# Optimization experiments

Measured on AMD Instinct MI355X. Metric: run time of the kernel, lower is better.

## Reference

```python
import jax, jax.numpy as jnp
import numpy as np

NUM_HEADS = 8
LN_EPS = 1e-5


def _avg_pool_mat(n_in, n_out):
    # torch adaptive_avg_pool windows: start=floor(i*n_in/n_out), end=ceil((i+1)*n_in/n_out)
    M = np.zeros((n_out, n_in), dtype=np.float32)
    for i in range(n_out):
        s = (i * n_in) // n_out
        e = -((-(i + 1) * n_in) // n_out)
        M[i, s:e] = 1.0 / (e - s)
    return jnp.asarray(M)


def _adaptive_avg_pool(x, out_hw):
    # separable mean over rectangular windows: [B,C,H,W] -> [B,C,out,out]
    Mh = _avg_pool_mat(x.shape[2], out_hw)
    Mw = _avg_pool_mat(x.shape[3], out_hw)
    return jnp.einsum('bchw,ph,qw->bcpq', x, Mh, Mw)


def _max_pool(x, oh, ow):
    # exact (divisible) adaptive max pool
    B, C, H, W = x.shape
    assert H % oh == 0 and W % ow == 0
    return x.reshape(B, C, oh, H // oh, ow, W // ow).max(axis=(3, 5))


def _conv1x1_res(t, w, b):
    # t + Conv2d(1x1)(t); w is [C_in, C_out]
    return t + jnp.einsum('bchw,cd->bdhw', t, w) + b[None, :, None, None]


def _tokens(t):
    B, C = t.shape[:2]
    return t.reshape(B, C, -1).transpose(0, 2, 1)  # [B, hw, C]


def setup_inputs():
    B, L, C = 8, 1024, 512
    H = W = 64
    key = jax.random.key(0)
    ks = jax.random.split(key, 16)
    n = lambda k, s, sc=0.02: jax.random.normal(k, s, jnp.float32) * sc
    return dict(
        x=jax.random.normal(ks[0], (B, H * W, C), jnp.float32),
        m=jax.random.normal(ks[1], (B, L, C), jnp.float32),
        w_s1=n(ks[2], (C, C)), b_s1=n(ks[3], (C,)),
        w_s2=n(ks[4], (C, C)), b_s2=n(ks[5], (C,)),
        w_s3=n(ks[6], (C, C)), b_s3=n(ks[7], (C,)),
        w_s4=n(ks[8], (C, C)), b_s4=n(ks[9], (C,)),
        w_mx=n(ks[10], (C, C)), b_mx=n(ks[11], (C,)),
        ln_g=jnp.ones((C,), jnp.float32), ln_b=jnp.zeros((C,), jnp.float32),
        Wq=n(ks[12], (C, C)), Wkv=n(ks[13], (C, 2 * C)),
        Wp=n(ks[14], (C, C)), bp=n(ks[15], (C,)),
        H=H, W=W, patch_size=16,
    )


def reference(x, m, w_s1, b_s1, w_s2, b_s2, w_s3, b_s3, w_s4, b_s4,
              w_mx, b_mx, ln_g, ln_b, Wq, Wkv, Wp, bp, H, W, patch_size):
    B, L, C = m.shape
    nh = NUM_HEADS
    d = C // nh
    scale = d ** -0.5

    q = (m @ Wq).reshape(B, L, nh, d).transpose(0, 2, 1, 3)  # [B,nh,L,d]

    x_ = x.transpose(0, 2, 1).reshape(B, C, H, W)
    s1 = _conv1x1_res(_adaptive_avg_pool(x_, round(H * 4 / 12)), w_s1, b_s1)
    s2 = _conv1x1_res(_adaptive_avg_pool(x_, round(H * 4 / 16)), w_s2, b_s2)
    s3 = _conv1x1_res(_adaptive_avg_pool(x_, round(H * 4 / 20)), w_s3, b_s3)
    s4 = _conv1x1_res(_adaptive_avg_pool(x_, round(H * 4 / 24)), w_s4, b_s4)
    mx = _conv1x1_res(_max_pool(x_, H * 4 // patch_size, W * 4 // patch_size), w_mx, b_mx)

    p = jnp.concatenate([_tokens(s1), _tokens(s2), _tokens(s3), _tokens(s4), _tokens(mx)], axis=1)
    mu = p.mean(-1, keepdims=True)
    var = ((p - mu) ** 2).mean(-1, keepdims=True)
    p = (p - mu) / jnp.sqrt(var + LN_EPS) * ln_g + ln_b

    kv_in = jnp.concatenate([p, m], axis=1)  # [B, N_p+L, C]
    kv = (kv_in @ Wkv).reshape(B, -1, 2, nh, d)
    k = kv[:, :, 0].transpose(0, 2, 1, 3)  # [B,nh,N,d]
    v = kv[:, :, 1].transpose(0, 2, 1, 3)

    attn = jax.nn.softmax(jnp.einsum('bhld,bhnd->bhln', q, k) * scale, axis=-1)
    out = jnp.einsum('bhln,bhnd->bhld', attn, v).transpose(0, 2, 1, 3).reshape(B, L, C)
    out = out @ Wp + bp
    return out, mx
```

## Files before the change

### kernel.cpp

```cpp
#include <hip/hip_runtime.h>

typedef unsigned short u16;
typedef __attribute__((ext_vector_type(8))) short bf16x8;
typedef __attribute__((ext_vector_type(4))) float f32x4;
typedef __attribute__((ext_vector_type(16))) float f32x16;
typedef int i32x2 __attribute__((ext_vector_type(2)));

__device__ __forceinline__ float bf2f(u16 u) {
  union { unsigned int i; float f; } x; x.i = ((unsigned int)u) << 16; return x.f;
}
__device__ __forceinline__ u16 f2bf(float f) {
  union { float f; unsigned int i; } x; x.f = f;
  unsigned int r = x.i + 0x7fffu + ((x.i >> 16) & 1u);
  return (u16)(r >> 16);
}

#define CFENCE() asm volatile("" ::: "memory")

__device__ __forceinline__ unsigned cvtpk_bf16(float lo, float hi) {
  unsigned r;
  asm("v_cvt_pk_bf16_f32 %0, %1, %2" : "=v"(r) : "v"(lo), "v"(hi));
  return r;
}

__global__ __launch_bounds__(256) void k_pool(
    const float* __restrict__ x, u16* __restrict__ pool,
    const float* __restrict__ m, u16* __restrict__ mb)
{
  int blk = blockIdx.x;
  if (blk >= 9944) {
    size_t i = ((size_t)(blk - 9944) * 256 + threadIdx.x) * 8;
    float4 a = *(const float4*)(m + i);
    float4 b = *(const float4*)(m + i + 4);
    ushort4 u0, u1;
    u0.x = f2bf(a.x); u0.y = f2bf(a.y); u0.z = f2bf(a.z); u0.w = f2bf(a.w);
    u1.x = f2bf(b.x); u1.y = f2bf(b.y); u1.z = f2bf(b.z); u1.w = f2bf(b.w);
    *(ushort4*)(mb + i) = u0;
    *(ushort4*)(mb + i + 4) = u1;
    return;
  }
  int b = blk / 1243;
  int tok = blk - b * 1243;
  int c = threadIdx.x;
  const float* xb = x + (size_t)b * 4096 * 512;
  float r0, r1;
  if (tok >= 987) {
    int t = tok - 987;
    int oh = t >> 4, ow = t & 15;
    float m0 = -1e38f, m1 = -1e38f;
    for (int hh = 0; hh < 4; hh++)
      for (int ww = 0; ww < 4; ww++) {
        const float* px = xb + (size_t)((oh * 4 + hh) * 64 + ow * 4 + ww) * 512 + c;
        m0 = fmaxf(m0, px[0]);
        m1 = fmaxf(m1, px[256]);
      }
    r0 = m0; r1 = m1;
  } else {
    int n, t;
    if (tok < 441)      { n = 21; t = tok; }
    else if (tok < 697) { n = 16; t = tok - 441; }
    else if (tok < 866) { n = 13; t = tok - 697; }
    else                { n = 11; t = tok - 866; }
    int oh = t / n, ow = t - oh * n;
    int h0 = (oh * 64) / n, h1 = ((oh + 1) * 64 + n - 1) / n;
    int w0 = (ow * 64) / n, w1 = ((ow + 1) * 64 + n - 1) / n;
    float inv = 1.0f / (float)((h1 - h0) * (w1 - w0));
    float s0 = 0.f, s1 = 0.f;
    for (int hh = h0; hh < h1; hh++)
      for (int ww = w0; ww < w1; ww++) {
        const float* px = xb + (size_t)(hh * 64 + ww) * 512 + c;
        s0 += px[0];
        s1 += px[256];
      }
    r0 = s0 * inv; r1 = s1 * inv;
  }
  u16* dst = pool + (size_t)(b * 1243 + tok) * 512 + c;
  dst[0]   = f2bf(r0);
  dst[256] = f2bf(r1);
}

__global__ __launch_bounds__(256) void k_wt8(
    const float* w0, const float* w1, const float* w2, const float* w3,
    const float* w4, const float* w5, const float* w6, const float* w7,
    u16* __restrict__ wt_base)
{
  int z = blockIdx.z;
  int N = (z == 6) ? 1024 : 512;
  if (N == 512 && blockIdx.x >= 16) return;
  const float* W =
      z == 0 ? w0 : z == 1 ? w1 : z == 2 ? w2 : z == 3 ? w3 :
      z == 4 ? w4 : z == 5 ? w5 : z == 6 ? w6 : w7;
  size_t doff = (z <= 5) ? (size_t)z * 262144
                         : (z == 6 ? (size_t)6 * 262144 : (size_t)6 * 262144 + 524288);
  u16* Wt = wt_base + doff;

  __shared__ float tile[32][33];
  int n0 = blockIdx.x * 32, k0 = blockIdx.y * 32;
  int t = threadIdx.x;
  int rr = t >> 5, cc = t & 31;
#pragma unroll
  for (int ps = 0; ps < 4; ps++)
    tile[ps * 8 + rr][cc] = W[(size_t)(k0 + ps * 8 + rr) * N + n0 + cc];
  __syncthreads();
#pragma unroll
  for (int ps = 0; ps < 4; ps++)
    Wt[(size_t)(n0 + ps * 8 + rr) * 512 + k0 + cc] = f2bf(tile[cc][ps * 8 + rr]);
}

template <class EPI>
__device__ __forceinline__ void gemm_core(
    const u16* __restrict__ Az, const u16* __restrict__ Bt,
    int M, int K, int m0, int n0, EPI&& epi)
{
  __shared__ __align__(16) u16 As[128][40];
  __shared__ __align__(16) u16 Bs[128][40];

  const int tid = threadIdx.x;
  const int lane = tid & 63, wv = tid >> 6;
  const int quad = lane >> 4, l15 = lane & 15;
  const int wm = (wv >> 1) * 64, wn = (wv & 1) * 64;

  f32x4 acc[4][4];
#pragma unroll
  for (int i = 0; i < 4; i++)
#pragma unroll
    for (int j = 0; j < 4; j++) acc[i][j] = (f32x4){0.f, 0.f, 0.f, 0.f};

  const int srow = tid >> 1;
  const int scol = (tid & 1) * 16;
  const bool aok = (m0 + srow) < M;
  const u16* ag = Az + (size_t)(m0 + srow) * K + scol;
  const u16* bg = Bt + (size_t)(n0 + srow) * K + scol;

  uint4 a0 = {0, 0, 0, 0}, a1 = {0, 0, 0, 0}, b0, b1;
  if (aok) { a0 = *(const uint4*)ag; a1 = *(const uint4*)(ag + 8); }
  b0 = *(const uint4*)bg;
  b1 = *(const uint4*)(bg + 8);

  for (int k0 = 0; k0 < K; k0 += 32) {
    CFENCE();
    __builtin_amdgcn_s_barrier();
    asm volatile("s_waitcnt vmcnt(0)" ::: "memory");
    *(uint4*)&As[srow][scol]     = a0;
    *(uint4*)&As[srow][scol + 8] = a1;
    *(uint4*)&Bs[srow][scol]     = b0;
    *(uint4*)&Bs[srow][scol + 8] = b1;
    if (k0 + 32 < K) {
      if (aok) { a0 = *(const uint4*)(ag + k0 + 32); a1 = *(const uint4*)(ag + k0 + 40); }
      b0 = *(const uint4*)(bg + k0 + 32);
      b1 = *(const uint4*)(bg + k0 + 40);
    }
    asm volatile("s_waitcnt lgkmcnt(0)" ::: "memory");
    __builtin_amdgcn_s_barrier();
    CFENCE();

    bf16x8 af[4];
#pragma unroll
    for (int i = 0; i < 4; i++)
      af[i] = *(const bf16x8*)&As[wm + i * 16 + l15][quad * 8];
#pragma unroll
    for (int j = 0; j < 4; j++) {
      bf16x8 bfj = *(const bf16x8*)&Bs[wn + j * 16 + l15][quad * 8];
#pragma unroll
      for (int i = 0; i < 4; i++)
        acc[i][j] = __builtin_amdgcn_mfma_f32_16x16x32_bf16(af[i], bfj, acc[i][j], 0, 0, 0);
    }
  }

#pragma unroll
  for (int i = 0; i < 4; i++) {
    int rb = m0 + wm + i * 16 + quad * 4;
#pragma unroll
    for (int j = 0; j < 4; j++) {
      int col = n0 + wn + j * 16 + l15;
#pragma unroll
      for (int r = 0; r < 4; r++) {
        int row = rb + r;
        if (row >= M) continue;
        epi(row, col, acc[i][j][r]);
      }
    }
  }
}

__global__ __launch_bounds__(256) void k_gemm_f32(
    const u16* __restrict__ A, long long a_bs, const u16* __restrict__ Bt,
    const float* __restrict__ bias, float* __restrict__ C, long long c_bs,
    int M, int N, int K)
{
  const u16* Az = A + (size_t)blockIdx.z * a_bs;
  float* Cz = C + (size_t)blockIdx.z * c_bs;
  gemm_core(Az, Bt, M, K, blockIdx.y * 128, blockIdx.x * 128,
            [&](int row, int col, float v) {
              Cz[(size_t)row * N + col] = v + bias[col];
            });
}

__global__ __launch_bounds__(256) void k_gemm_big(
    const u16* __restrict__ mb, const u16* __restrict__ p,
    const u16* __restrict__ wqkv, const u16* __restrict__ wkv,
    u16* __restrict__ q, u16* __restrict__ KV)
{
  int y = blockIdx.y, z = blockIdx.z;
  if (y < 8) {
    const u16* Az = mb + (size_t)z * (1024 * 512);
    u16* qz  = q  + (size_t)z * (1024 * 512);
    u16* kvz = KV + (size_t)(z * 2267 + 1243) * 1024;
    gemm_core(Az, wqkv, 1024, 512, y * 128, blockIdx.x * 128,
              [&](int row, int col, float v) {
                u16 bv = f2bf(v);
                if (col < 512) qz[(size_t)row * 512 + col] = bv;
                else           kvz[(size_t)row * 1024 + (col - 512)] = bv;
              });
  } else {
    if (blockIdx.x >= 8) return;
    const u16* Az = p + (size_t)z * (1243 * 512);
    u16* kvz = KV + (size_t)z * 2267 * 1024;
    gemm_core(Az, wkv, 1243, 512, (y - 8) * 128, blockIdx.x * 128,
              [&](int row, int col, float v) {
                kvz[(size_t)row * 1024 + col] = f2bf(v);
              });
  }
}

__global__ __launch_bounds__(256) void k_conv_seg(
    const u16* __restrict__ pool, const u16* __restrict__ wts,
    const float* b0, const float* b1, const float* b2, const float* b3,
    const float* b4, u16* __restrict__ p, float* __restrict__ out2)
{
  int y = blockIdx.y, bz = blockIdx.z;
  int s, m0;
  if (y < 4)      { s = 0; m0 = y * 128; }
  else if (y < 6) { s = 1; m0 = (y - 4) * 128; }
  else if (y < 8) { s = 2; m0 = (y - 6) * 128; }
  else if (y < 9) { s = 3; m0 = 0; }
  else            { s = 4; m0 = (y - 9) * 128; }
  int t0  = s == 0 ? 0 : s == 1 ? 441 : s == 2 ? 697 : s == 3 ? 866 : 987;
  int cnt = s == 0 ? 441 : s == 1 ? 256 : s == 2 ? 169 : s == 3 ? 121 : 256;
  const float* bias = s == 0 ? b0 : s == 1 ? b1 : s == 2 ? b2 : s == 3 ? b3 : b4;
  size_t base = (size_t)bz * (1243 * 512) + (size_t)t0 * 512;
  const u16* Az = pool + base;
  u16* Cz = p + base;
  gemm_core(Az, wts + (size_t)s * 262144, cnt, 512, m0, blockIdx.x * 128,
            [&](int row, int col, float v) {
              v += bias[col] + bf2f(Az[(size_t)row * 512 + col]);
              Cz[(size_t)row * 512 + col] = f2bf(v);
              if (s == 4)
                out2[((size_t)(bz * 512 + col)) * 256 + row] = v;
            });
}

__global__ __launch_bounds__(256) void k_ln(
    u16* __restrict__ p, const float* __restrict__ g, const float* __restrict__ bb)
{
  __shared__ float red[8];
  size_t row = blockIdx.x;
  u16* pr = p + row * 512;
  int t = threadIdx.x;
  float v0 = bf2f(pr[t]), v1 = bf2f(pr[t + 256]);
  float s = v0 + v1;
#pragma unroll
  for (int off = 1; off < 64; off <<= 1) s += __shfl_xor(s, off);
  int wave = t >> 6;
  if ((t & 63) == 0) red[wave] = s;
  __syncthreads();
  float mean = (red[0] + red[1] + red[2] + red[3]) * (1.f / 512.f);
  float d0 = v0 - mean, d1 = v1 - mean;
  float s2 = d0 * d0 + d1 * d1;
#pragma unroll
  for (int off = 1; off < 64; off <<= 1) s2 += __shfl_xor(s2, off);
  if ((t & 63) == 0) red[4 + wave] = s2;
  __syncthreads();
  float var = (red[4] + red[5] + red[6] + red[7]) * (1.f / 512.f);
  float rstd = rsqrtf(var + 1e-5f);
  pr[t]       = f2bf(d0 * rstd * g[t]       + bb[t]);
  pr[t + 256] = f2bf(d1 * rstd * g[t + 256] + bb[t + 256]);
}

__global__ __launch_bounds__(256) void k_attn_mfma(
    const u16* __restrict__ qb, const u16* __restrict__ KV,
    u16* __restrict__ outb)
{
  __shared__ __align__(16) u16 Ks_[64][68];
  __shared__ __align__(16) u16 Vt_[64][68];

  const int bid = blockIdx.x;
  const int qt = bid >> 6;
  const int hb = bid & 63;
  const int h = hb & 7, b = hb >> 3;
  const int tid = threadIdx.x;
  const int lane = tid & 63, wv = tid >> 6;
  const int l31 = lane & 31, hl = lane >> 5;

  const u16* kvb = KV + (size_t)b * 2267 * 1024;
  const int kr = tid >> 2, kc = (tid & 3) * 16;
  const int vp = tid & 31, vo = tid >> 5;

  uint4 k0r = {0,0,0,0}, k1r = {0,0,0,0}, vra = {0,0,0,0}, vrb = {0,0,0,0};
  auto load_tile = [&](int n0) {
    k0r = (uint4){0,0,0,0}; k1r = (uint4){0,0,0,0};
    vra = (uint4){0,0,0,0}; vrb = (uint4){0,0,0,0};
    if (n0 + kr < 2267) {
      const u16* s = kvb + (size_t)(n0 + kr) * 1024 + h * 64 + kc;
      k0r = *(const uint4*)s;
      k1r = *(const uint4*)(s + 8);
    }
    int na = n0 + 2 * vp;
    const u16* s = kvb + (size_t)na * 1024 + 512 + h * 64 + vo * 8;
    if (na < 2267)     vra = *(const uint4*)s;
    if (na + 1 < 2267) vrb = *(const uint4*)(s + 1024);
  };

  load_tile(0);
  bf16x8 qf[4];
  {
    const u16* qrow = qb + (size_t)(b * 1024 + qt * 128 + wv * 32 + l31) * 512
                    + h * 64 + hl * 8;
    qf[0] = *(const bf16x8*)(qrow);
    qf[1] = *(const bf16x8*)(qrow + 16);
    qf[2] = *(const bf16x8*)(qrow + 32);
    qf[3] = *(const bf16x8*)(qrow + 48);
  }

  float l_acc = 0.f;
  f32x16 o0, o1;
#pragma unroll
  for (int i = 0; i < 16; i++) { o0[i] = 0.f; o1[i] = 0.f; }

  __syncthreads();

  for (int n0 = 0; n0 < 2267; n0 += 64) {
    CFENCE();
    __builtin_amdgcn_s_barrier();
    asm volatile("s_waitcnt vmcnt(0)" ::: "memory");
    *(uint4*)&Ks_[kr][kc]     = k0r;
    *(uint4*)&Ks_[kr][kc + 8] = k1r;
    {
      const unsigned* pa = (const unsigned*)&vra;
      const unsigned* pb = (const unsigned*)&vrb;
#pragma unroll
      for (int i = 0; i < 4; i++) {
        unsigned lo = __builtin_amdgcn_perm(pb[i], pa[i], 0x05040100u);
        unsigned hi = __builtin_amdgcn_perm(pb[i], pa[i], 0x07060302u);
        *(unsigned*)&Vt_[vo * 8 + 2 * i][2 * vp]     = lo;
        *(unsigned*)&Vt_[vo * 8 + 2 * i + 1][2 * vp] = hi;
      }
    }
    if (n0 + 64 < 2267) load_tile(n0 + 64);
    asm volatile("s_waitcnt lgkmcnt(0)" ::: "memory");
    __builtin_amdgcn_s_barrier();
    CFENCE();

#pragma unroll
    for (int s = 0; s < 2; s++) {
      f32x16 sacc;
#pragma unroll
      for (int i = 0; i < 16; i++) sacc[i] = 0.f;
      __builtin_amdgcn_s_setprio(1);
#pragma unroll
      for (int c = 0; c < 4; c++) {
        bf16x8 kf = *(const bf16x8*)&Ks_[s * 32 + l31][c * 16 + hl * 8];
        sacc = __builtin_amdgcn_mfma_f32_32x32x16_bf16(kf, qf[c], sacc, 0, 0, 0);
      }
      __builtin_amdgcn_s_setprio(0);

      unsigned w[8];
#pragma unroll
      for (int j = 0; j < 8; j++) {
        float e0 = __builtin_amdgcn_exp2f(fminf(sacc[2 * j]     * 0.18033688f, 43.28f));
        float e1 = __builtin_amdgcn_exp2f(fminf(sacc[2 * j + 1] * 0.18033688f, 43.28f));
        l_acc += e0 + e1;
        w[j] = cvtpk_bf16(e0, e1);
      }
      i32x2 s02 = __builtin_amdgcn_permlane32_swap((int)w[0], (int)w[2], false, false);
      i32x2 s13 = __builtin_amdgcn_permlane32_swap((int)w[1], (int)w[3], false, false);
      i32x2 s46 = __builtin_amdgcn_permlane32_swap((int)w[4], (int)w[6], false, false);
      i32x2 s57 = __builtin_amdgcn_permlane32_swap((int)w[5], (int)w[7], false, false);
      uint4 f0, f1;
      f0.x = (unsigned)s02[0]; f0.y = (unsigned)s13[0];
      f0.z = (unsigned)s02[1]; f0.w = (unsigned)s13[1];
      f1.x = (unsigned)s46[0]; f1.y = (unsigned)s57[0];
      f1.z = (unsigned)s46[1]; f1.w = (unsigned)s57[1];
      bf16x8 ap0 = __builtin_bit_cast(bf16x8, f0);
      bf16x8 ap1 = __builtin_bit_cast(bf16x8, f1);

      __builtin_amdgcn_s_setprio(1);
      {
        bf16x8 v00 = *(const bf16x8*)&Vt_[l31][s * 32 + hl * 8];
        bf16x8 v01 = *(const bf16x8*)&Vt_[l31][s * 32 + 16 + hl * 8];
        bf16x8 v10 = *(const bf16x8*)&Vt_[32 + l31][s * 32 + hl * 8];
        bf16x8 v11 = *(const bf16x8*)&Vt_[32 + l31][s * 32 + 16 + hl * 8];
        o0 = __builtin_amdgcn_mfma_f32_32x32x16_bf16(ap0, v00, o0, 0, 0, 0);
        o0 = __builtin_amdgcn_mfma_f32_32x32x16_bf16(ap1, v01, o0, 0, 0, 0);
        o1 = __builtin_amdgcn_mfma_f32_32x32x16_bf16(ap0, v10, o1, 0, 0, 0);
        o1 = __builtin_amdgcn_mfma_f32_32x32x16_bf16(ap1, v11, o1, 0, 0, 0);
      }
      __builtin_amdgcn_s_setprio(0);
    }
  }

  l_acc += __shfl_xor(l_acc, 32);

#pragma unroll
  for (int r = 0; r < 16; r++) {
    int qr = (r & 3) + 8 * (r >> 2) + 4 * hl;
    float lq = __shfl(l_acc, qr);
    float inv = 1.f / fmaxf(lq - 37.f, 1e-20f);
    size_t row = (size_t)(b * 1024 + qt * 128 + wv * 32 + qr);
    outb[row * 512 + h * 64 + l31]      = f2bf(o0[r] * inv);
    outb[row * 512 + h * 64 + 32 + l31] = f2bf(o1[r] * inv);
  }
}

extern "C" void kernel_launch(void* const* d_in, const int* in_sizes, int n_in,
                              void* d_out, int out_size, void* d_ws, size_t ws_size,
                              hipStream_t stream)
{
  const float* x = (const float*)d_in[0];
  const float* m = (const float*)d_in[1];
  const float* ln_g = (const float*)d_in[12];
  const float* ln_b = (const float*)d_in[13];
  const float* Wq   = (const float*)d_in[14];
  const float* Wkv  = (const float*)d_in[15];
  const float* Wp   = (const float*)d_in[16];
  const float* bp   = (const float*)d_in[17];
  float* out = (float*)d_out;

  u16* pool = (u16*)d_ws;
  u16* p    = pool + 5091328;
  u16* q    = p + 5091328;
  u16* KV   = q + 4194304;
  u16* mb   = KV + 18571264;
  u16* wt_s = mb + 4194304;
  u16* attn_out = pool;

  k_wt8<<<dim3(32, 16, 8), 256, 0, stream>>>(
      (const float*)d_in[2], (const float*)d_in[4], (const float*)d_in[6],
      (const float*)d_in[8], (const float*)d_in[10], Wq, Wkv, Wp, wt_s);

  k_pool<<<11992, 256, 0, stream>>>(x, pool, m, mb);

  k_conv_seg<<<dim3(4, 11, 8), 256, 0, stream>>>(
      pool, wt_s, (const float*)d_in[3], (const float*)d_in[5],
      (const float*)d_in[7], (const float*)d_in[9], (const float*)d_in[11],
      p, out + 4194304);

  k_ln<<<9944, 256, 0, stream>>>(p, ln_g, ln_b);

  k_gemm_big<<<dim3(12, 18, 8), 256, 0, stream>>>(
      mb, p, wt_s + 5 * 262144, wt_s + 6 * 262144, q, KV);

  k_attn_mfma<<<512, 256, 0, stream>>>(q, KV, attn_out);

  k_gemm_f32<<<dim3(4, 8, 8), 256, 0, stream>>>(attn_out, (long long)1024 * 512,
                                                wt_s + 6 * 262144 + 524288, bp,
                                                out, (long long)1024 * 512,
                                                1024, 512, 512);
  (void)in_sizes; (void)n_in; (void)out_size; (void)ws_size;
}
```

Measured before the change: 372.0 us.

## Split attention key tiles across wave pairs with LDS reduction of partial outputs

The attention kernel now runs 512 threads per block. Each of four query-row groups is handled by two waves, and each wave of a pair processes one 32-key half of every 64-key tile. This doubles the waves available per block, which gives more latency hiding on a 512-block grid. In exchange it adds a final LDS reduction of the partial O accumulators and row sums, and extra barriers. Global loads are also reshaped so that each thread loads less per tile.

```diff
diff --git a/kernel.cpp b/kernel.cpp
--- a/kernel.cpp
+++ b/kernel.cpp
@@ -277,12 +277,13 @@
   pr[t + 256] = f2bf(d1 * rstd * g[t + 256] + bb[t + 256]);
 }
 
-__global__ __launch_bounds__(256) void k_attn_mfma(
+__global__ __launch_bounds__(512) void k_attn_mfma(
     const u16* __restrict__ qb, const u16* __restrict__ KV,
     u16* __restrict__ outb)
 {
-  __shared__ __align__(16) u16 Ks_[64][68];
-  __shared__ __align__(16) u16 Vt_[64][68];
+  __shared__ __align__(16) u16 smem[16640];
+  u16 (*Ks_)[68] = (u16 (*)[68])smem;
+  u16 (*Vt_)[68] = (u16 (*)[68])(smem + 4352);
 
   const int bid = blockIdx.x;
   const int qt = bid >> 6;
@@ -290,31 +291,31 @@
   const int h = hb & 7, b = hb >> 3;
   const int tid = threadIdx.x;
   const int lane = tid & 63, wv = tid >> 6;
+  const int qw = wv >> 1, kw = wv & 1;
   const int l31 = lane & 31, hl = lane >> 5;
 
   const u16* kvb = KV + (size_t)b * 2267 * 1024;
-  const int kr = tid >> 2, kc = (tid & 3) * 16;
-  const int vp = tid & 31, vo = tid >> 5;
-
-  uint4 k0r = {0,0,0,0}, k1r = {0,0,0,0}, vra = {0,0,0,0}, vrb = {0,0,0,0};
+  const int kr = tid >> 3, kc = (tid & 7) * 8;
+  const int vp = tid & 31, vc = (tid >> 5) * 4;
+
+  uint4 kreg = {0, 0, 0, 0};
+  uint2 vra = {0, 0}, vrb = {0, 0};
   auto load_tile = [&](int n0) {
-    k0r = (uint4){0,0,0,0}; k1r = (uint4){0,0,0,0};
-    vra = (uint4){0,0,0,0}; vrb = (uint4){0,0,0,0};
-    if (n0 + kr < 2267) {
-      const u16* s = kvb + (size_t)(n0 + kr) * 1024 + h * 64 + kc;
-      k0r = *(const uint4*)s;
-      k1r = *(const uint4*)(s + 8);
-    }
+    kreg = (uint4){0, 0, 0, 0};
+    vra = (uint2){0, 0};
+    vrb = (uint2){0, 0};
+    if (n0 + kr < 2267)
+      kreg = *(const uint4*)(kvb + (size_t)(n0 + kr) * 1024 + h * 64 + kc);
     int na = n0 + 2 * vp;
-    const u16* s = kvb + (size_t)na * 1024 + 512 + h * 64 + vo * 8;
-    if (na < 2267)     vra = *(const uint4*)s;
-    if (na + 1 < 2267) vrb = *(const uint4*)(s + 1024);
+    const u16* s = kvb + (size_t)na * 1024 + 512 + h * 64 + vc;
+    if (na < 2267)     vra = *(const uint2*)s;
+    if (na + 1 < 2267) vrb = *(const uint2*)(s + 1024);
   };
 
   load_tile(0);
   bf16x8 qf[4];
   {
-    const u16* qrow = qb + (size_t)(b * 1024 + qt * 128 + wv * 32 + l31) * 512
+    const u16* qrow = qb + (size_t)(b * 1024 + qt * 128 + qw * 32 + l31) * 512
                     + h * 64 + hl * 8;
     qf[0] = *(const bf16x8*)(qrow);
     qf[1] = *(const bf16x8*)(qrow + 16);
@@ -333,82 +334,94 @@
     CFENCE();
     __builtin_amdgcn_s_barrier();
     asm volatile("s_waitcnt vmcnt(0)" ::: "memory");
-    *(uint4*)&Ks_[kr][kc]     = k0r;
-    *(uint4*)&Ks_[kr][kc + 8] = k1r;
+    *(uint4*)&Ks_[kr][kc] = kreg;
     {
-      const unsigned* pa = (const unsigned*)&vra;
-      const unsigned* pb = (const unsigned*)&vrb;
-#pragma unroll
-      for (int i = 0; i < 4; i++) {
-        unsigned lo = __builtin_amdgcn_perm(pb[i], pa[i], 0x05040100u);
-        unsigned hi = __builtin_amdgcn_perm(pb[i], pa[i], 0x07060302u);
-        *(unsigned*)&Vt_[vo * 8 + 2 * i][2 * vp]     = lo;
-        *(unsigned*)&Vt_[vo * 8 + 2 * i + 1][2 * vp] = hi;
-      }
+      unsigned lo0 = __builtin_amdgcn_perm(vrb.x, vra.x, 0x05040100u);
+      unsigned hi0 = __builtin_amdgcn_perm(vrb.x, vra.x, 0x07060302u);
+      unsigned lo1 = __builtin_amdgcn_perm(vrb.y, vra.y, 0x05040100u);
+      unsigned hi1 = __builtin_amdgcn_perm(vrb.y, vra.y, 0x07060302u);
+      *(unsigned*)&Vt_[vc + 0][2 * vp] = lo0;
+      *(unsigned*)&Vt_[vc + 1][2 * vp] = hi0;
+      *(unsigned*)&Vt_[vc + 2][2 * vp] = lo1;
+      *(unsigned*)&Vt_[vc + 3][2 * vp] = hi1;
     }
     if (n0 + 64 < 2267) load_tile(n0 + 64);
     asm volatile("s_waitcnt lgkmcnt(0)" ::: "memory");
     __builtin_amdgcn_s_barrier();
     CFENCE();
 
-#pragma unroll
-    for (int s = 0; s < 2; s++) {
-      f32x16 sacc;
-#pragma unroll
-      for (int i = 0; i < 16; i++) sacc[i] = 0.f;
-      __builtin_amdgcn_s_setprio(1);
-#pragma unroll
-      for (int c = 0; c < 4; c++) {
-        bf16x8 kf = *(const bf16x8*)&Ks_[s * 32 + l31][c * 16 + hl * 8];
-        sacc = __builtin_amdgcn_mfma_f32_32x32x16_bf16(kf, qf[c], sacc, 0, 0, 0);
-      }
-      __builtin_amdgcn_s_setprio(0);
-
-      unsigned w[8];
-#pragma unroll
-      for (int j = 0; j < 8; j++) {
-        float e0 = __builtin_amdgcn_exp2f(fminf(sacc[2 * j]     * 0.18033688f, 43.28f));
-        float e1 = __builtin_amdgcn_exp2f(fminf(sacc[2 * j + 1] * 0.18033688f, 43.28f));
-        l_acc += e0 + e1;
-        w[j] = cvtpk_bf16(e0, e1);
-      }
-      i32x2 s02 = __builtin_amdgcn_permlane32_swap((int)w[0], (int)w[2], false, false);
-      i32x2 s13 = __builtin_amdgcn_permlane32_swap((int)w[1], (int)w[3], false, false);
-      i32x2 s46 = __builtin_amdgcn_permlane32_swap((int)w[4], (int)w[6], false, false);
-      i32x2 s57 = __builtin_amdgcn_permlane32_swap((int)w[5], (int)w[7], false, false);
-      uint4 f0, f1;
-      f0.x = (unsigned)s02[0]; f0.y = (unsigned)s13[0];
-      f0.z = (unsigned)s02[1]; f0.w = (unsigned)s13[1];
-      f1.x = (unsigned)s46[0]; f1.y = (unsigned)s57[0];
-      f1.z = (unsigned)s46[1]; f1.w = (unsigned)s57[1];
-      bf16x8 ap0 = __builtin_bit_cast(bf16x8, f0);
-      bf16x8 ap1 = __builtin_bit_cast(bf16x8, f1);
-
-      __builtin_amdgcn_s_setprio(1);
-      {
-        bf16x8 v00 = *(const bf16x8*)&Vt_[l31][s * 32 + hl * 8];
-        bf16x8 v01 = *(const bf16x8*)&Vt_[l31][s * 32 + 16 + hl * 8];
-        bf16x8 v10 = *(const bf16x8*)&Vt_[32 + l31][s * 32 + hl * 8];
-        bf16x8 v11 = *(const bf16x8*)&Vt_[32 + l31][s * 32 + 16 + hl * 8];
-        o0 = __builtin_amdgcn_mfma_f32_32x32x16_bf16(ap0, v00, o0, 0, 0, 0);
-        o0 = __builtin_amdgcn_mfma_f32_32x32x16_bf16(ap1, v01, o0, 0, 0, 0);
-        o1 = __builtin_amdgcn_mfma_f32_32x32x16_bf16(ap0, v10, o1, 0, 0, 0);
-        o1 = __builtin_amdgcn_mfma_f32_32x32x16_bf16(ap1, v11, o1, 0, 0, 0);
-      }
-      __builtin_amdgcn_s_setprio(0);
-    }
+    f32x16 sacc;
+#pragma unroll
+    for (int i = 0; i < 16; i++) sacc[i] = 0.f;
+    __builtin_amdgcn_s_setprio(1);
+#pragma unroll
+    for (int c = 0; c < 4; c++) {
+      bf16x8 kf = *(const bf16x8*)&Ks_[kw * 32 + l31][c * 16 + hl * 8];
+      sacc = __builtin_amdgcn_mfma_f32_32x32x16_bf16(kf, qf[c], sacc, 0, 0, 0);
+    }
+    __builtin_amdgcn_s_setprio(0);
+
+    unsigned w[8];
+#pragma unroll
+    for (int j = 0; j < 8; j++) {
+      float e0 = __builtin_amdgcn_exp2f(fminf(sacc[2 * j]     * 0.18033688f, 43.28f));
+      float e1 = __builtin_amdgcn_exp2f(fminf(sacc[2 * j + 1] * 0.18033688f, 43.28f));
+      l_acc += e0 + e1;
+      w[j] = cvtpk_bf16(e0, e1);
+    }
+    i32x2 s02 = __builtin_amdgcn_permlane32_swap((int)w[0], (int)w[2], false, false);
+    i32x2 s13 = __builtin_amdgcn_permlane32_swap((int)w[1], (int)w[3], false, false);
+    i32x2 s46 = __builtin_amdgcn_permlane32_swap((int)w[4], (int)w[6], false, false);
+    i32x2 s57 = __builtin_amdgcn_permlane32_swap((int)w[5], (int)w[7], false, false);
+    uint4 f0, f1;
+    f0.x = (unsigned)s02[0]; f0.y = (unsigned)s13[0];
+    f0.z = (unsigned)s02[1]; f0.w = (unsigned)s13[1];
+    f1.x = (unsigned)s46[0]; f1.y = (unsigned)s57[0];
+    f1.z = (unsigned)s46[1]; f1.w = (unsigned)s57[1];
+    bf16x8 ap0 = __builtin_bit_cast(bf16x8, f0);
+    bf16x8 ap1 = __builtin_bit_cast(bf16x8, f1);
+
+    __builtin_amdgcn_s_setprio(1);
+    {
+      bf16x8 v00 = *(const bf16x8*)&Vt_[l31][kw * 32 + hl * 8];
+      bf16x8 v01 = *(const bf16x8*)&Vt_[l31][kw * 32 + 16 + hl * 8];
+      bf16x8 v10 = *(const bf16x8*)&Vt_[32 + l31][kw * 32 + hl * 8];
+      bf16x8 v11 = *(const bf16x8*)&Vt_[32 + l31][kw * 32 + 16 + hl * 8];
+      o0 = __builtin_amdgcn_mfma_f32_32x32x16_bf16(ap0, v00, o0, 0, 0, 0);
+      o0 = __builtin_amdgcn_mfma_f32_32x32x16_bf16(ap1, v01, o0, 0, 0, 0);
+      o1 = __builtin_amdgcn_mfma_f32_32x32x16_bf16(ap0, v10, o1, 0, 0, 0);
+      o1 = __builtin_amdgcn_mfma_f32_32x32x16_bf16(ap1, v11, o1, 0, 0, 0);
+    }
+    __builtin_amdgcn_s_setprio(0);
   }
 
   l_acc += __shfl_xor(l_acc, 32);
 
-#pragma unroll
-  for (int r = 0; r < 16; r++) {
-    int qr = (r & 3) + 8 * (r >> 2) + 4 * hl;
-    float lq = __shfl(l_acc, qr);
-    float inv = 1.f / fmaxf(lq - 37.f, 1e-20f);
-    size_t row = (size_t)(b * 1024 + qt * 128 + wv * 32 + qr);
-    outb[row * 512 + h * 64 + l31]      = f2bf(o0[r] * inv);
-    outb[row * 512 + h * 64 + 32 + l31] = f2bf(o1[r] * inv);
+  float* Op = (float*)smem;
+  float* Lp = (float*)smem + 8192;
+  __syncthreads();
+  if (kw == 1) {
+#pragma unroll
+    for (int r = 0; r < 16; r++) {
+      int qr = (r & 3) + 8 * (r >> 2) + 4 * hl;
+      Op[(qw * 32 + qr) * 64 + l31]      = o0[r];
+      Op[(qw * 32 + qr) * 64 + 32 + l31] = o1[r];
+    }
+    if (lane < 32) Lp[qw * 32 + l31] = l_acc;
+  }
+  __syncthreads();
+  if (kw == 0) {
+#pragma unroll
+    for (int r = 0; r < 16; r++) {
+      int qr = (r & 3) + 8 * (r >> 2) + 4 * hl;
+      float lt = __shfl(l_acc, qr) + Lp[qw * 32 + qr] - 37.f;
+      float inv = 1.f / fmaxf(lt, 1e-20f);
+      size_t row = (size_t)(b * 1024 + qt * 128 + qw * 32 + qr);
+      outb[row * 512 + h * 64 + l31] =
+          f2bf((o0[r] + Op[(qw * 32 + qr) * 64 + l31]) * inv);
+      outb[row * 512 + h * 64 + 32 + l31] =
+          f2bf((o1[r] + Op[(qw * 32 + qr) * 64 + 32 + l31]) * inv);
+    }
   }
 }
 
@@ -450,7 +463,7 @@
   k_gemm_big<<<dim3(12, 18, 8), 256, 0, stream>>>(
       mb, p, wt_s + 5 * 262144, wt_s + 6 * 262144, q, KV);
 
-  k_attn_mfma<<<512, 256, 0, stream>>>(q, KV, attn_out);
+  k_attn_mfma<<<512, 512, 0, stream>>>(q, KV, attn_out);
 
   k_gemm_f32<<<dim3(4, 8, 8), 256, 0, stream>>>(attn_out, (long long)1024 * 512,
                                                 wt_s + 6 * 262144 + 524288, bp,
```

After: 453.9 us. 22.0% more time.

## Split attention over two key halves with a separate combine kernel

Applied to the files above, without the earlier changes.

The attention kernel now splits the key/value sequence into two halves, doubling the grid from 512 to 1024 blocks. Each block writes unnormalized fp32 partial outputs and row sums to workspace buffers. A new combine kernel adds the two partials, applies the padding-corrected normalization and writes bf16 output. This is meant to raise occupancy and parallelism across the CUs, at the cost of an extra launch and roughly 64MB of extra fp32 traffic.

```diff
diff --git a/kernel.cpp b/kernel.cpp
--- a/kernel.cpp
+++ b/kernel.cpp
@@ -279,18 +279,22 @@
 
 __global__ __launch_bounds__(256) void k_attn_mfma(
     const u16* __restrict__ qb, const u16* __restrict__ KV,
-    u16* __restrict__ outb)
+    float* __restrict__ PO0, float* __restrict__ PO1, float* __restrict__ PL)
 {
   __shared__ __align__(16) u16 Ks_[64][68];
   __shared__ __align__(16) u16 Vt_[64][68];
 
   const int bid = blockIdx.x;
-  const int qt = bid >> 6;
   const int hb = bid & 63;
+  const int qt = (bid >> 6) & 7;
+  const int half = bid >> 9;
   const int h = hb & 7, b = hb >> 3;
   const int tid = threadIdx.x;
   const int lane = tid & 63, wv = tid >> 6;
   const int l31 = lane & 31, hl = lane >> 5;
+
+  const int nbase = half * 1152;
+  const int nend  = half ? 2267 : 1152;
 
   const u16* kvb = KV + (size_t)b * 2267 * 1024;
   const int kr = tid >> 2, kc = (tid & 3) * 16;
@@ -311,7 +315,7 @@
     if (na + 1 < 2267) vrb = *(const uint4*)(s + 1024);
   };
 
-  load_tile(0);
+  load_tile(nbase);
   bf16x8 qf[4];
   {
     const u16* qrow = qb + (size_t)(b * 1024 + qt * 128 + wv * 32 + l31) * 512
@@ -329,7 +333,7 @@
 
   __syncthreads();
 
-  for (int n0 = 0; n0 < 2267; n0 += 64) {
+  for (int n0 = nbase; n0 < nend; n0 += 64) {
     CFENCE();
     __builtin_amdgcn_s_barrier();
     asm volatile("s_waitcnt vmcnt(0)" ::: "memory");
@@ -346,7 +350,7 @@
         *(unsigned*)&Vt_[vo * 8 + 2 * i + 1][2 * vp] = hi;
       }
     }
-    if (n0 + 64 < 2267) load_tile(n0 + 64);
+    if (n0 + 64 < nend) load_tile(n0 + 64);
     asm volatile("s_waitcnt lgkmcnt(0)" ::: "memory");
     __builtin_amdgcn_s_barrier();
     CFENCE();
@@ -401,15 +405,37 @@
 
   l_acc += __shfl_xor(l_acc, 32);
 
+  float* PO = half ? PO1 : PO0;
 #pragma unroll
   for (int r = 0; r < 16; r++) {
     int qr = (r & 3) + 8 * (r >> 2) + 4 * hl;
-    float lq = __shfl(l_acc, qr);
-    float inv = 1.f / fmaxf(lq - 37.f, 1e-20f);
     size_t row = (size_t)(b * 1024 + qt * 128 + wv * 32 + qr);
-    outb[row * 512 + h * 64 + l31]      = f2bf(o0[r] * inv);
-    outb[row * 512 + h * 64 + 32 + l31] = f2bf(o1[r] * inv);
-  }
+    PO[row * 512 + h * 64 + l31]      = o0[r];
+    PO[row * 512 + h * 64 + 32 + l31] = o1[r];
+  }
+  if (hl == 0)
+    PL[half * 65536 + ((b * 8 + h) << 10) + qt * 128 + wv * 32 + l31] = l_acc;
+}
+
+__global__ __launch_bounds__(256) void k_combine(
+    const float* __restrict__ PO0, const float* __restrict__ PO1,
+    const float* __restrict__ PL, u16* __restrict__ dst)
+{
+  size_t idx = ((size_t)blockIdx.x * 256 + threadIdx.x) * 4;
+  int b = (int)(idx >> 19);
+  int q = (int)((idx >> 9) & 1023);
+  int h = (int)((idx & 511) >> 6);
+  int li = ((b * 8 + h) << 10) + q;
+  float l = PL[li] + PL[65536 + li] - 37.f;
+  float inv = 1.f / fmaxf(l, 1e-20f);
+  float4 a = *(const float4*)(PO0 + idx);
+  float4 c = *(const float4*)(PO1 + idx);
+  ushort4 o;
+  o.x = f2bf((a.x + c.x) * inv);
+  o.y = f2bf((a.y + c.y) * inv);
+  o.z = f2bf((a.z + c.z) * inv);
+  o.w = f2bf((a.w + c.w) * inv);
+  *(ushort4*)(dst + idx) = o;
 }
 
 extern "C" void kernel_launch(void* const* d_in, const int* in_sizes, int n_in,
@@ -432,7 +458,11 @@
   u16* KV   = q + 4194304;
   u16* mb   = KV + 18571264;
   u16* wt_s = mb + 4194304;
-  u16* attn_out = pool;
+
+  float* PO0 = out;
+  float* PO1 = (float*)pool;
+  float* PL  = (float*)wt_s;
+  u16* attn_out = mb;
 
   k_wt8<<<dim3(32, 16, 8), 256, 0, stream>>>(
       (const float*)d_in[2], (const float*)d_in[4], (const float*)d_in[6],
@@ -450,7 +480,9 @@
   k_gemm_big<<<dim3(12, 18, 8), 256, 0, stream>>>(
       mb, p, wt_s + 5 * 262144, wt_s + 6 * 262144, q, KV);
 
-  k_attn_mfma<<<512, 256, 0, stream>>>(q, KV, attn_out);
+  k_attn_mfma<<<1024, 256, 0, stream>>>(q, KV, PO0, PO1, PL);
+
+  k_combine<<<4096, 256, 0, stream>>>(PO0, PO1, PL, attn_out);
 
   k_gemm_f32<<<dim3(4, 8, 8), 256, 0, stream>>>(attn_out, (long long)1024 * 512,
                                                 wt_s + 6 * 262144 + 524288, bp,
```

Result: no change. 375.3 us (+0.9%).
